# Optimization experiments

Hardware: AMD Instinct MI355X
Metric: run time of the kernel (lower is better)

## Reference

```python
import jax, jax.numpy as jnp
import numpy as np

B, H, S, DK = 2, 16, 2048, 64


def setup_inputs() -> dict:
    key = jax.random.key(0)
    k1, k2, k3, k4 = jax.random.split(key, 4)
    Q = jax.random.normal(k1, (B, H, S, DK), dtype=jnp.float32)
    K = jax.random.normal(k2, (B, H, S, DK), dtype=jnp.float32)
    V = jax.random.normal(k3, (B, H, S, DK), dtype=jnp.float32)
    attn_mask = jax.random.randint(k4, (B, 1, S, S), 0, 2).astype(jnp.bool_)
    return {"Q": Q, "K": K, "V": V, "attn_mask": attn_mask}


def reference(Q, K, V, attn_mask):
    d_k = Q.shape[-1]
    scale = 1.0 / jnp.sqrt(jnp.asarray(d_k, dtype=Q.dtype))
    # scores: [B,H,S,S]
    scores = jnp.einsum('bhqd,bhkd->bhqk', Q, K) * scale
    scores = jnp.where(attn_mask, jnp.asarray(-1e9, dtype=scores.dtype), scores)
    attn = jax.nn.softmax(scores, axis=-1)
    # dropout in eval mode (identity) for deterministic reference
    return jnp.einsum('bhqk,bhkd->bhqd', attn, V)
```

## Files before the change

### kernel.cpp

```cpp
#include <hip/hip_runtime.h>
#include <hip/hip_bf16.h>

#define Bdim 2
#define Hdim 16
#define Sdim 2048
#define Ddim 64
#define KVBLK 64
#define NT (Sdim / KVBLK)
#define WQ 32
#define NWAVE 4
#define QTILE (WQ * NWAVE)
#define QSCL (0.125f * 1.44269504088896f)
#define SCALE 0.125f
#define BUFE 8192
#define VOFF 4096

typedef __bf16 bf16x8 __attribute__((ext_vector_type(8)));
typedef float  f32x4  __attribute__((ext_vector_type(4)));
typedef float  f32x16 __attribute__((ext_vector_type(16)));
typedef unsigned u32x4 __attribute__((ext_vector_type(4)));

__device__ __forceinline__ void gll16(const __bf16* g, __bf16* l) {
  __builtin_amdgcn_global_load_lds(
      (const __attribute__((address_space(1))) void*)g,
      (__attribute__((address_space(3))) void*)l, 16, 0, 0);
}
__device__ __forceinline__ unsigned cvtpk_raw(float lo, float hi) {
  unsigned r;
  asm("v_cvt_pk_bf16_f32 %0, %1, %2" : "=v"(r) : "v"(lo), "v"(hi));
  return r;
}
template <bool SW>
__device__ __forceinline__ unsigned pko(float a, float b) {
  return SW ? cvtpk_raw(b, a) : cvtpk_raw(a, b);
}
__device__ __forceinline__ unsigned cvtpk(float a, float b, bool sw) {
  const float lo = sw ? b : a;
  const float hi = sw ? a : b;
  return cvtpk_raw(lo, hi);
}
template <bool SW>
__device__ __forceinline__ void packAll(const float (&sv0)[16],
                                        const float (&sv1)[16],
                                        unsigned (&pw)[16]) {
#pragma unroll
  for (int ks = 0; ks < 4; ++ks) {
    const int rb = 8 * (ks & 1);
    if (ks < 2) {
      pw[ks * 4 + 0] = pko<SW>(sv0[rb + 0], sv0[rb + 1]);
      pw[ks * 4 + 1] = pko<SW>(sv0[rb + 2], sv0[rb + 3]);
      pw[ks * 4 + 2] = pko<SW>(sv0[rb + 4], sv0[rb + 5]);
      pw[ks * 4 + 3] = pko<SW>(sv0[rb + 6], sv0[rb + 7]);
    } else {
      pw[ks * 4 + 0] = pko<SW>(sv1[rb + 0], sv1[rb + 1]);
      pw[ks * 4 + 1] = pko<SW>(sv1[rb + 2], sv1[rb + 3]);
      pw[ks * 4 + 2] = pko<SW>(sv1[rb + 4], sv1[rb + 5]);
      pw[ks * 4 + 3] = pko<SW>(sv1[rb + 6], sv1[rb + 7]);
    }
  }
}

__global__ __launch_bounds__(256) void pack_mask_kernel(
    const void* __restrict__ mask, unsigned long long* __restrict__ packed) {
  const int nwords = Bdim * Sdim * (Sdim / 64);
  const unsigned* m32 = (const unsigned*)mask;
  const unsigned char* m8 = (const unsigned char*)mask;
  int gid = blockIdx.x * blockDim.x + threadIdx.x;
  int lane = gid & 63;
  int wid = gid >> 6;
  int nwaves = (gridDim.x * blockDim.x) >> 6;

  bool isBytes = __any(m32[lane] > 1u);

  for (int w = wid; w < nwords; w += nwaves) {
    int v = isBytes ? (int)m8[(size_t)w * 64 + lane]
                    : (int)m32[(size_t)w * 64 + lane];
    unsigned long long bal = __ballot(v != 0);
    if (lane == 0) packed[w] = bal;
  }
}

__global__ __launch_bounds__(256) void prep_kv(
    const float* __restrict__ K, const float* __restrict__ V,
    __bf16* __restrict__ Kb, __bf16* __restrict__ Vt) {
  __shared__ __bf16 tile[64][72];
  const int bh = blockIdx.y, st = blockIdx.x;
  const int t = threadIdx.x;
  const int r = t >> 2, c0 = (t & 3) << 4;
  {
    const float* ks = K + ((size_t)bh * Sdim + st * 64 + r) * Ddim + c0;
    bf16x8 o0, o1;
#pragma unroll
    for (int j = 0; j < 8; ++j) o0[j] = (__bf16)ks[j];
#pragma unroll
    for (int j = 0; j < 8; ++j) o1[j] = (__bf16)ks[8 + j];
    __bf16* kd = Kb + ((size_t)bh * Sdim + st * 64 + r) * Ddim + c0;
    *(bf16x8*)kd = o0;
    *(bf16x8*)(kd + 8) = o1;
  }
  {
    const float* vs = V + ((size_t)bh * Sdim + st * 64 + r) * Ddim + c0;
#pragma unroll
    for (int j = 0; j < 16; ++j) tile[r][c0 + j] = (__bf16)vs[j];
  }
  __syncthreads();
  {
    const int d = t >> 2, s0 = (t & 3) << 4;
    __bf16 o[16];
#pragma unroll
    for (int j = 0; j < 16; ++j) o[j] = tile[s0 + j][d];
    __bf16* dst = Vt + ((size_t)bh * Ddim + d) * Sdim + st * 64 + s0;
    *(bf16x8*)dst = *(bf16x8*)&o[0];
    *(bf16x8*)(dst + 8) = *(bf16x8*)&o[8];
  }
}

__global__ __launch_bounds__(256, 2) void attn4(
    const float* __restrict__ Q, const __bf16* __restrict__ Kb,
    const __bf16* __restrict__ Vt,
    const unsigned long long* __restrict__ maskP, float* __restrict__ Out) {
  __shared__ alignas(16) __bf16 sm[3 * BUFE];

  const int tid = threadIdx.x;
  const int lane = tid & 63;
  const int w = tid >> 6;
  const int l31 = lane & 31;
  const int hi = lane >> 5;
  const int rsw = l31 & 7;

  const int bid = blockIdx.x;
  const int bh = bid & 31;
  const int qt = bid >> 5;
  const int b = bh >> 4;
  const int qrow = qt * QTILE + w * WQ + l31;

  const __bf16* Kbase = Kb + (size_t)bh * Sdim * Ddim;
  const __bf16* Vbase = Vt + (size_t)bh * (size_t)Ddim * Sdim;
  const unsigned long long* mp =
      maskP + ((size_t)b * Sdim + qrow) * (Sdim / 64);

  const bool sw = (cvtpk_raw(0.0f, 1.0f) & 0xFFFFu) != 0u;

  bf16x8 qf[4];
  {
    const float* qs = Q + ((size_t)bh * Sdim + qrow) * Ddim;
#pragma unroll
    for (int step = 0; step < 4; ++step) {
      const int d0 = step * 16 + hi * 8;
      float4 a = *(const float4*)(qs + d0);
      float4 c = *(const float4*)(qs + d0 + 4);
      u32x4 f;
      f[0] = cvtpk(a.x * QSCL, a.y * QSCL, sw);
      f[1] = cvtpk(a.z * QSCL, a.w * QSCL, sw);
      f[2] = cvtpk(c.x * QSCL, c.y * QSCL, sw);
      f[3] = cvtpk(c.z * QSCL, c.w * QSCL, sw);
      qf[step] = __builtin_bit_cast(bf16x8, f);
    }
  }

  const int srow = 16 * w + (lane >> 3);
  const int sblk = (lane & 7) ^ ((lane >> 3) & 7);
  const int dstw = w * 1024;

#define STAGE(off_, kt_)                                                        \
  do {                                                                          \
    const __bf16* kp_ = Kbase + ((size_t)(kt_)*KVBLK + srow) * Ddim + sblk * 8; \
    gll16(kp_, &sm[(off_) + dstw]);                                             \
    gll16(kp_ + 8 * Ddim, &sm[(off_) + dstw + 512]);                            \
    const __bf16* vp_ =                                                         \
        Vbase + (size_t)srow * Sdim + (size_t)(kt_)*KVBLK + sblk * 8;           \
    gll16(vp_, &sm[(off_) + VOFF + dstw]);                                      \
    gll16(vp_ + 8 * Sdim, &sm[(off_) + VOFF + dstw + 512]);                     \
  } while (0)

  f32x16 otA = {0,0,0,0,0,0,0,0,0,0,0,0,0,0,0,0};
  f32x16 otB = {0,0,0,0,0,0,0,0,0,0,0,0,0,0,0,0};
  float lrow = 0.f;

  unsigned long long mwCur = mp[0];
  STAGE(0, 0);
  int rdOff = 0, stOff = BUFE;

#pragma unroll 1
  for (int kt = 0; kt < NT; ++kt) {
    const unsigned long long mwNext = mp[kt + 1 < NT ? kt + 1 : NT - 1];
    if (kt + 1 < NT) {
      STAGE(stOff, kt + 1);
      asm volatile("s_waitcnt vmcnt(5)" ::: "memory");
    } else {
      asm volatile("s_waitcnt vmcnt(1)" ::: "memory");
    }
    __builtin_amdgcn_s_barrier();
    __builtin_amdgcn_sched_barrier(0);

    f32x16 st0 = {0,0,0,0,0,0,0,0,0,0,0,0,0,0,0,0};
    f32x16 st1 = {0,0,0,0,0,0,0,0,0,0,0,0,0,0,0,0};
    __builtin_amdgcn_s_setprio(1);
#pragma unroll
    for (int step = 0; step < 4; ++step) {
      bf16x8 kf = *(const bf16x8*)&sm[rdOff + l31 * 64 + (((step * 2 + hi) ^ rsw) << 3)];
      st0 = __builtin_amdgcn_mfma_f32_32x32x16_bf16(kf, qf[step], st0, 0, 0, 0);
    }
#pragma unroll
    for (int step = 0; step < 4; ++step) {
      bf16x8 kf = *(const bf16x8*)&sm[rdOff + (32 + l31) * 64 + (((step * 2 + hi) ^ rsw) << 3)];
      st1 = __builtin_amdgcn_mfma_f32_32x32x16_bf16(kf, qf[step], st1, 0, 0, 0);
    }
    __builtin_amdgcn_s_setprio(0);

    float sv0[16], sv1[16];
    const unsigned w0s = ((unsigned)mwCur) >> (hi * 4);
    const unsigned w1s = ((unsigned)(mwCur >> 32)) >> (hi * 4);
#pragma unroll
    for (int r = 0; r < 16; ++r) {
      const int cr = (r & 3) + 8 * (r >> 2);
      const float e0 = __builtin_amdgcn_exp2f(st0[r]);
      const float e1 = __builtin_amdgcn_exp2f(st1[r]);
      sv0[r] = ((w0s >> cr) & 1u) ? 0.f : e0;
      sv1[r] = ((w1s >> cr) & 1u) ? 0.f : e1;
    }

    float s8[8];
#pragma unroll
    for (int j = 0; j < 8; ++j)
      s8[j] = (sv0[j] + sv0[j + 8]) + (sv1[j] + sv1[j + 8]);
    lrow += ((s8[0] + s8[4]) + (s8[1] + s8[5])) +
            ((s8[2] + s8[6]) + (s8[3] + s8[7]));

    unsigned pw[16];
    if (!sw) packAll<false>(sv0, sv1, pw);
    else     packAll<true>(sv0, sv1, pw);
    bf16x8 pb[4];
#pragma unroll
    for (int ks = 0; ks < 4; ++ks) {
      const unsigned W0 = pw[ks * 4 + 0], W1 = pw[ks * 4 + 1];
      const unsigned X0 = pw[ks * 4 + 2], X1 = pw[ks * 4 + 3];
      const unsigned s1 = hi ? W0 : X0;
      const unsigned s2 = hi ? W1 : X1;
      const unsigned r1 = __shfl_xor(s1, 32, 64);
      const unsigned r2 = __shfl_xor(s2, 32, 64);
      u32x4 wv;
      wv[0] = hi ? r1 : W0;
      wv[1] = hi ? r2 : W1;
      wv[2] = hi ? X0 : r1;
      wv[3] = hi ? X1 : r2;
      pb[ks] = __builtin_bit_cast(bf16x8, wv);
    }

    __builtin_amdgcn_s_setprio(1);
#pragma unroll
    for (int ks = 0; ks < 4; ++ks) {
      bf16x8 vf = *(const bf16x8*)&sm[rdOff + VOFF + l31 * 64 + (((ks * 2 + hi) ^ rsw) << 3)];
      otA = __builtin_amdgcn_mfma_f32_32x32x16_bf16(vf, pb[ks], otA, 0, 0, 0);
    }
#pragma unroll
    for (int ks = 0; ks < 4; ++ks) {
      bf16x8 vf = *(const bf16x8*)&sm[rdOff + VOFF + (32 + l31) * 64 + (((ks * 2 + hi) ^ rsw) << 3)];
      otB = __builtin_amdgcn_mfma_f32_32x32x16_bf16(vf, pb[ks], otB, 0, 0, 0);
    }
    __builtin_amdgcn_s_setprio(0);

    mwCur = mwNext;
    rdOff = stOff;
    stOff = (stOff == 2 * BUFE) ? 0 : stOff + BUFE;
  }
#undef STAGE

  lrow += __shfl_xor(lrow, 32, 64);
  const float inv = 1.f / (lrow + 1e-30f);
  float* orow = Out + ((size_t)bh * Sdim + qrow) * Ddim;
#pragma unroll
  for (int g = 0; g < 4; ++g) {
    const int d0 = 8 * g + 4 * hi;
    float4 va = {otA[4 * g] * inv, otA[4 * g + 1] * inv,
                 otA[4 * g + 2] * inv, otA[4 * g + 3] * inv};
    float4 vb = {otB[4 * g] * inv, otB[4 * g + 1] * inv,
                 otB[4 * g + 2] * inv, otB[4 * g + 3] * inv};
    *(float4*)(orow + d0) = va;
    *(float4*)(orow + 32 + d0) = vb;
  }
}

__global__ __launch_bounds__(256) void attn_fallback(
    const float* __restrict__ Q, const float* __restrict__ K,
    const float* __restrict__ V, const void* __restrict__ maskRaw,
    float* __restrict__ Out) {
  __shared__ alignas(16) __bf16 Kl[KVBLK * Ddim];
  __shared__ alignas(16) __bf16 Vts[Ddim * KVBLK];
  __shared__ alignas(16) __bf16 Pl[4][16 * 64];

  const int tid = threadIdx.x;
  const int lane = tid & 63;
  const int w = tid >> 6;
  const int lhi = lane >> 4;
  const int llo = lane & 15;

  const int qt = blockIdx.x;
  const int bh = blockIdx.y;
  const int b = bh >> 4;
  const int qbase = qt * 64;

  const float* Qp = Q + (size_t)bh * Sdim * Ddim;
  const float* Kp = K + (size_t)bh * Sdim * Ddim;
  const float* Vp = V + (size_t)bh * Sdim * Ddim;

  bool maskBytes = __any(((const unsigned*)maskRaw)[lane] > 1u);

  bf16x8 qf0, qf1;
  {
    const int qr = qbase + w * 16 + llo;
    const float* src = Qp + (size_t)qr * Ddim + lhi * 8;
#pragma unroll
    for (int i = 0; i < 8; ++i) qf0[i] = (__bf16)(src[i] * SCALE);
#pragma unroll
    for (int i = 0; i < 8; ++i) qf1[i] = (__bf16)(src[32 + i] * SCALE);
  }

  f32x4 acc[4] = {{0.f,0.f,0.f,0.f},{0.f,0.f,0.f,0.f},
                  {0.f,0.f,0.f,0.f},{0.f,0.f,0.f,0.f}};
  float mrow[4], lrw[4];
#pragma unroll
  for (int r = 0; r < 4; ++r) { mrow[r] = -3.0e38f; lrw[r] = 0.f; }

  for (int kt = 0; kt < NT; ++kt) {
    __syncthreads();
    {
      int r = tid >> 2;
      int c0 = (tid & 3) << 4;
      const float* ks = Kp + (size_t)(kt * KVBLK + r) * Ddim + c0;
      const float* vs = Vp + (size_t)(kt * KVBLK + r) * Ddim + c0;
      float kv[16], vv[16];
#pragma unroll
      for (int j = 0; j < 4; ++j) {
        *(float4*)(&kv[j * 4]) = *(const float4*)(ks + j * 4);
        *(float4*)(&vv[j * 4]) = *(const float4*)(vs + j * 4);
      }
      const int swzK = (r & 7) << 3;
      bf16x8 k0v, k1v;
#pragma unroll
      for (int j = 0; j < 8; ++j) { k0v[j] = (__bf16)kv[j]; k1v[j] = (__bf16)kv[8 + j]; }
      *(bf16x8*)&Kl[r * 64 + (c0 ^ swzK)] = k0v;
      *(bf16x8*)&Kl[r * 64 + ((c0 + 8) ^ swzK)] = k1v;
#pragma unroll
      for (int j = 0; j < 16; ++j) {
        int d = c0 + j;
        Vts[d * 64 + (r ^ ((d & 7) << 3))] = (__bf16)vv[j];
      }
    }
    __syncthreads();

    float sv[4][4];
#pragma unroll
    for (int cb = 0; cb < 4; ++cb) {
      int krow = cb * 16 + llo;
      int swz = (krow & 7) << 3;
      bf16x8 kf0 = *(const bf16x8*)&Kl[krow * 64 + ((lhi * 8) ^ swz)];
      bf16x8 kf1 = *(const bf16x8*)&Kl[krow * 64 + ((32 + lhi * 8) ^ swz)];
      f32x4 s = {0.f, 0.f, 0.f, 0.f};
      s = __builtin_amdgcn_mfma_f32_16x16x32_bf16(qf0, kf0, s, 0, 0, 0);
      s = __builtin_amdgcn_mfma_f32_16x16x32_bf16(qf1, kf1, s, 0, 0, 0);
#pragma unroll
      for (int r = 0; r < 4; ++r) {
        size_t q = qbase + w * 16 + lhi * 4 + r;
        size_t k = (size_t)kt * KVBLK + cb * 16 + llo;
        size_t idx = ((size_t)b * Sdim + q) * Sdim + k;
        bool masked = maskBytes ? (((const unsigned char*)maskRaw)[idx] != 0)
                                : (((const int*)maskRaw)[idx] != 0);
        sv[cb][r] = masked ? -1e9f : s[r];
      }
    }

    float corr[4], tsum[4];
#pragma unroll
    for (int r = 0; r < 4; ++r) {
      float mx = fmaxf(fmaxf(sv[0][r], sv[1][r]), fmaxf(sv[2][r], sv[3][r]));
#pragma unroll
      for (int off = 1; off < 16; off <<= 1)
        mx = fmaxf(mx, __shfl_xor(mx, off, 64));
      float mnew = fmaxf(mrow[r], mx);
      corr[r] = __expf(mrow[r] - mnew);
      mrow[r] = mnew;
      tsum[r] = 0.f;
    }
#pragma unroll
    for (int cb = 0; cb < 4; ++cb) {
#pragma unroll
      for (int r = 0; r < 4; ++r) {
        float p = __expf(sv[cb][r] - mrow[r]);
        tsum[r] += p;
        int row = lhi * 4 + r;
        int col = cb * 16 + llo;
        Pl[w][row * 64 + (col ^ ((row & 7) << 3))] = (__bf16)p;
      }
    }
#pragma unroll
    for (int r = 0; r < 4; ++r) {
      float s = tsum[r];
#pragma unroll
      for (int off = 1; off < 16; off <<= 1)
        s += __shfl_xor(s, off, 64);
      lrw[r] = lrw[r] * corr[r] + s;
#pragma unroll
      for (int db = 0; db < 4; ++db) acc[db][r] *= corr[r];
    }
    asm volatile("s_waitcnt lgkmcnt(0)" ::: "memory");

    bf16x8 pf0 = *(const bf16x8*)&Pl[w][llo * 64 + ((lhi * 8) ^ ((llo & 7) << 3))];
    bf16x8 pf1 = *(const bf16x8*)&Pl[w][llo * 64 + ((32 + lhi * 8) ^ ((llo & 7) << 3))];
#pragma unroll
    for (int db = 0; db < 4; ++db) {
      int d = db * 16 + llo;
      int swz = (d & 7) << 3;
      bf16x8 vf0 = *(const bf16x8*)&Vts[d * 64 + ((lhi * 8) ^ swz)];
      bf16x8 vf1 = *(const bf16x8*)&Vts[d * 64 + ((32 + lhi * 8) ^ swz)];
      acc[db] = __builtin_amdgcn_mfma_f32_16x16x32_bf16(pf0, vf0, acc[db], 0, 0, 0);
      acc[db] = __builtin_amdgcn_mfma_f32_16x16x32_bf16(pf1, vf1, acc[db], 0, 0, 0);
    }
  }

#pragma unroll
  for (int r = 0; r < 4; ++r) {
    float inv = 1.f / lrw[r];
    int q = qbase + w * 16 + lhi * 4 + r;
    float* dst = Out + ((size_t)bh * Sdim + q) * Ddim + llo;
#pragma unroll
    for (int db = 0; db < 4; ++db) dst[db * 16] = acc[db][r] * inv;
  }
}

extern "C" void kernel_launch(void* const* d_in, const int* in_sizes, int n_in,
                              void* d_out, int out_size, void* d_ws, size_t ws_size,
                              hipStream_t stream) {
  const float* Q = (const float*)d_in[0];
  const float* K = (const float*)d_in[1];
  const float* V = (const float*)d_in[2];
  const void* mask = d_in[3];
  float* out = (float*)d_out;

  const size_t packed_bytes =
      (size_t)Bdim * Sdim * (Sdim / 64) * sizeof(unsigned long long);
  const size_t tensor_bf16 = (size_t)Bdim * Hdim * Sdim * Ddim * 2;

  if (ws_size >= packed_bytes + 2 * tensor_bf16) {
    unsigned long long* packed = (unsigned long long*)d_ws;
    __bf16* Kb = (__bf16*)((char*)d_ws + packed_bytes);
    __bf16* Vt = (__bf16*)((char*)d_ws + packed_bytes + tensor_bf16);
    pack_mask_kernel<<<512, 256, 0, stream>>>(mask, packed);
    prep_kv<<<dim3(Sdim / 64, Bdim * Hdim), 256, 0, stream>>>(K, V, Kb, Vt);
    attn4<<<(Sdim / QTILE) * Bdim * Hdim, 256, 0, stream>>>(Q, Kb, Vt, packed, out);
  } else {
    attn_fallback<<<dim3(Sdim / 64, Bdim * Hdim), 256, 0, stream>>>(Q, K, V, mask, out);
  }
}
```

Baseline: 95.41 us.

## Merge prep kernels and unroll attention loop over four LDS buffers

After: 96.32 us. No clear change (+1.0%).

```diff
diff --git a/kernel.cpp b/kernel.cpp
--- a/kernel.cpp
+++ b/kernel.cpp
@@ -60,32 +60,33 @@
   }
 }
 
-__global__ __launch_bounds__(256) void pack_mask_kernel(
-    const void* __restrict__ mask, unsigned long long* __restrict__ packed) {
-  const int nwords = Bdim * Sdim * (Sdim / 64);
-  const unsigned* m32 = (const unsigned*)mask;
-  const unsigned char* m8 = (const unsigned char*)mask;
-  int gid = blockIdx.x * blockDim.x + threadIdx.x;
-  int lane = gid & 63;
-  int wid = gid >> 6;
-  int nwaves = (gridDim.x * blockDim.x) >> 6;
-
-  bool isBytes = __any(m32[lane] > 1u);
-
-  for (int w = wid; w < nwords; w += nwaves) {
-    int v = isBytes ? (int)m8[(size_t)w * 64 + lane]
-                    : (int)m32[(size_t)w * 64 + lane];
-    unsigned long long bal = __ballot(v != 0);
-    if (lane == 0) packed[w] = bal;
-  }
-}
-
-__global__ __launch_bounds__(256) void prep_kv(
+__global__ __launch_bounds__(256) void prep_all(
+    const void* __restrict__ mask, unsigned long long* __restrict__ packed,
     const float* __restrict__ K, const float* __restrict__ V,
     __bf16* __restrict__ Kb, __bf16* __restrict__ Vt) {
   __shared__ __bf16 tile[64][72];
-  const int bh = blockIdx.y, st = blockIdx.x;
   const int t = threadIdx.x;
+
+  if (blockIdx.x < 512) {
+    const int nwords = Bdim * Sdim * (Sdim / 64);
+    const unsigned* m32 = (const unsigned*)mask;
+    const unsigned char* m8 = (const unsigned char*)mask;
+    int gid = blockIdx.x * 256 + t;
+    int lane = gid & 63;
+    int wid = gid >> 6;
+    const int nwaves = 512 * 256 / 64;
+    bool isBytes = __any(m32[lane] > 1u);
+    for (int w = wid; w < nwords; w += nwaves) {
+      int v = isBytes ? (int)m8[(size_t)w * 64 + lane]
+                      : (int)m32[(size_t)w * 64 + lane];
+      unsigned long long bal = __ballot(v != 0);
+      if (lane == 0) packed[w] = bal;
+    }
+    return;
+  }
+
+  const int idx = blockIdx.x - 512;
+  const int bh = idx >> 5, st = idx & 31;
   const int r = t >> 2, c0 = (t & 3) << 4;
   {
     const float* ks = K + ((size_t)bh * Sdim + st * 64 + r) * Ddim + c0;
@@ -115,11 +116,11 @@
   }
 }
 
-__global__ __launch_bounds__(256, 2) void attn4(
+__global__ __launch_bounds__(256, 2) void attn5(
     const float* __restrict__ Q, const __bf16* __restrict__ Kb,
     const __bf16* __restrict__ Vt,
     const unsigned long long* __restrict__ maskP, float* __restrict__ Out) {
-  __shared__ alignas(16) __bf16 sm[3 * BUFE];
+  __shared__ alignas(16) __bf16 sm[4 * BUFE];
 
   const int tid = threadIdx.x;
   const int lane = tid & 63;
@@ -162,15 +163,12 @@
   const int sblk = (lane & 7) ^ ((lane >> 3) & 7);
   const int dstw = w * 1024;
 
-#define STAGE(off_, kt_)                                                        \
-  do {                                                                          \
-    const __bf16* kp_ = Kbase + ((size_t)(kt_)*KVBLK + srow) * Ddim + sblk * 8; \
-    gll16(kp_, &sm[(off_) + dstw]);                                             \
-    gll16(kp_ + 8 * Ddim, &sm[(off_) + dstw + 512]);                            \
-    const __bf16* vp_ =                                                         \
-        Vbase + (size_t)srow * Sdim + (size_t)(kt_)*KVBLK + sblk * 8;           \
-    gll16(vp_, &sm[(off_) + VOFF + dstw]);                                      \
-    gll16(vp_ + 8 * Sdim, &sm[(off_) + VOFF + dstw + 512]);                     \
+#define STAGE(OFFE, kp_, vp_)                                   \
+  do {                                                          \
+    gll16((kp_), &sm[(OFFE) + dstw]);                           \
+    gll16((kp_) + 8 * Ddim, &sm[(OFFE) + dstw + 512]);          \
+    gll16((vp_), &sm[(OFFE) + VOFF + dstw]);                    \
+    gll16((vp_) + 8 * Sdim, &sm[(OFFE) + VOFF + dstw + 512]);   \
   } while (0)
 
   f32x16 otA = {0,0,0,0,0,0,0,0,0,0,0,0,0,0,0,0};
@@ -178,92 +176,102 @@
   float lrow = 0.f;
 
   unsigned long long mwCur = mp[0];
-  STAGE(0, 0);
-  int rdOff = 0, stOff = BUFE;
+  {
+    const __bf16* kp0 = Kbase + (size_t)srow * Ddim + sblk * 8;
+    const __bf16* vp0 = Vbase + (size_t)srow * Sdim + sblk * 8;
+    STAGE(0, kp0, vp0);
+  }
+  const __bf16* kpS = Kbase + (size_t)(KVBLK + srow) * Ddim + sblk * 8;
+  const __bf16* vpS = Vbase + (size_t)srow * Sdim + KVBLK + sblk * 8;
+
+#define ITER(RD, ST, KTN, LAST)                                                \
+  do {                                                                         \
+    unsigned long long mwNext = 0;                                             \
+    if (!(LAST)) {                                                             \
+      mwNext = mp[(KTN)];                                                      \
+      STAGE((ST) * BUFE, kpS, vpS);                                            \
+      kpS += (size_t)KVBLK * Ddim;                                             \
+      vpS += KVBLK;                                                            \
+      asm volatile("s_waitcnt vmcnt(5)" ::: "memory");                         \
+    } else {                                                                   \
+      asm volatile("s_waitcnt vmcnt(0)" ::: "memory");                         \
+    }                                                                          \
+    __builtin_amdgcn_s_barrier();                                              \
+    __builtin_amdgcn_sched_barrier(0);                                         \
+    f32x16 st0 = {0,0,0,0,0,0,0,0,0,0,0,0,0,0,0,0};                            \
+    f32x16 st1 = {0,0,0,0,0,0,0,0,0,0,0,0,0,0,0,0};                            \
+    __builtin_amdgcn_s_setprio(1);                                             \
+    _Pragma("unroll") for (int step = 0; step < 4; ++step) {                   \
+      bf16x8 kf = *(const bf16x8*)&sm[(RD) * BUFE + l31 * 64 +                 \
+                                      (((step * 2 + hi) ^ rsw) << 3)];         \
+      st0 = __builtin_amdgcn_mfma_f32_32x32x16_bf16(kf, qf[step], st0, 0,0,0); \
+    }                                                                          \
+    _Pragma("unroll") for (int step = 0; step < 4; ++step) {                   \
+      bf16x8 kf = *(const bf16x8*)&sm[(RD) * BUFE + (32 + l31) * 64 +          \
+                                      (((step * 2 + hi) ^ rsw) << 3)];         \
+      st1 = __builtin_amdgcn_mfma_f32_32x32x16_bf16(kf, qf[step], st1, 0,0,0); \
+    }                                                                          \
+    __builtin_amdgcn_s_setprio(0);                                             \
+    float sv0[16], sv1[16];                                                    \
+    const unsigned w0s = ((unsigned)mwCur) >> (hi * 4);                        \
+    const unsigned w1s = ((unsigned)(mwCur >> 32)) >> (hi * 4);                \
+    _Pragma("unroll") for (int r = 0; r < 16; ++r) {                           \
+      const int cr = (r & 3) + 8 * (r >> 2);                                   \
+      const float e0 = __builtin_amdgcn_exp2f(st0[r]);                         \
+      const float e1 = __builtin_amdgcn_exp2f(st1[r]);                         \
+      sv0[r] = ((w0s >> cr) & 1u) ? 0.f : e0;                                  \
+      sv1[r] = ((w1s >> cr) & 1u) ? 0.f : e1;                                  \
+    }                                                                          \
+    float s8[8];                                                               \
+    _Pragma("unroll") for (int j = 0; j < 8; ++j)                              \
+      s8[j] = (sv0[j] + sv0[j + 8]) + (sv1[j] + sv1[j + 8]);                   \
+    lrow += ((s8[0] + s8[4]) + (s8[1] + s8[5])) +                              \
+            ((s8[2] + s8[6]) + (s8[3] + s8[7]));                               \
+    unsigned pw[16];                                                           \
+    if (!sw) packAll<false>(sv0, sv1, pw);                                     \
+    else     packAll<true>(sv0, sv1, pw);                                      \
+    bf16x8 pb[4];                                                              \
+    _Pragma("unroll") for (int ks = 0; ks < 4; ++ks) {                         \
+      const unsigned W0 = pw[ks * 4 + 0], W1 = pw[ks * 4 + 1];                 \
+      const unsigned X0 = pw[ks * 4 + 2], X1 = pw[ks * 4 + 3];                 \
+      const unsigned s1 = hi ? W0 : X0;                                        \
+      const unsigned s2 = hi ? W1 : X1;                                        \
+      const unsigned r1 = __shfl_xor(s1, 32, 64);                              \
+      const unsigned r2 = __shfl_xor(s2, 32, 64);                              \
+      u32x4 wv;                                                                \
+      wv[0] = hi ? r1 : W0;                                                    \
+      wv[1] = hi ? r2 : W1;                                                    \
+      wv[2] = hi ? X0 : r1;                                                    \
+      wv[3] = hi ? X1 : r2;                                                    \
+      pb[ks] = __builtin_bit_cast(bf16x8, wv);                                 \
+    }                                                                          \
+    __builtin_amdgcn_s_setprio(1);                                             \
+    _Pragma("unroll") for (int ks = 0; ks < 4; ++ks) {                         \
+      bf16x8 vf = *(const bf16x8*)&sm[(RD) * BUFE + VOFF + l31 * 64 +          \
+                                      (((ks * 2 + hi) ^ rsw) << 3)];           \
+      otA = __builtin_amdgcn_mfma_f32_32x32x16_bf16(vf, pb[ks], otA, 0,0,0);   \
+    }                                                                          \
+    _Pragma("unroll") for (int ks = 0; ks < 4; ++ks) {                         \
+      bf16x8 vf = *(const bf16x8*)&sm[(RD) * BUFE + VOFF + (32 + l31) * 64 +   \
+                                      (((ks * 2 + hi) ^ rsw) << 3)];           \
+      otB = __builtin_amdgcn_mfma_f32_32x32x16_bf16(vf, pb[ks], otB, 0,0,0);   \
+    }                                                                          \
+    __builtin_amdgcn_s_setprio(0);                                             \
+    if (!(LAST)) mwCur = mwNext;                                               \
+  } while (0)
 
 #pragma unroll 1
-  for (int kt = 0; kt < NT; ++kt) {
-    const unsigned long long mwNext = mp[kt + 1 < NT ? kt + 1 : NT - 1];
-    if (kt + 1 < NT) {
-      STAGE(stOff, kt + 1);
-      asm volatile("s_waitcnt vmcnt(5)" ::: "memory");
-    } else {
-      asm volatile("s_waitcnt vmcnt(1)" ::: "memory");
-    }
-    __builtin_amdgcn_s_barrier();
-    __builtin_amdgcn_sched_barrier(0);
-
-    f32x16 st0 = {0,0,0,0,0,0,0,0,0,0,0,0,0,0,0,0};
-    f32x16 st1 = {0,0,0,0,0,0,0,0,0,0,0,0,0,0,0,0};
-    __builtin_amdgcn_s_setprio(1);
-#pragma unroll
-    for (int step = 0; step < 4; ++step) {
-      bf16x8 kf = *(const bf16x8*)&sm[rdOff + l31 * 64 + (((step * 2 + hi) ^ rsw) << 3)];
-      st0 = __builtin_amdgcn_mfma_f32_32x32x16_bf16(kf, qf[step], st0, 0, 0, 0);
-    }
-#pragma unroll
-    for (int step = 0; step < 4; ++step) {
-      bf16x8 kf = *(const bf16x8*)&sm[rdOff + (32 + l31) * 64 + (((step * 2 + hi) ^ rsw) << 3)];
-      st1 = __builtin_amdgcn_mfma_f32_32x32x16_bf16(kf, qf[step], st1, 0, 0, 0);
-    }
-    __builtin_amdgcn_s_setprio(0);
-
-    float sv0[16], sv1[16];
-    const unsigned w0s = ((unsigned)mwCur) >> (hi * 4);
-    const unsigned w1s = ((unsigned)(mwCur >> 32)) >> (hi * 4);
-#pragma unroll
-    for (int r = 0; r < 16; ++r) {
-      const int cr = (r & 3) + 8 * (r >> 2);
-      const float e0 = __builtin_amdgcn_exp2f(st0[r]);
-      const float e1 = __builtin_amdgcn_exp2f(st1[r]);
-      sv0[r] = ((w0s >> cr) & 1u) ? 0.f : e0;
-      sv1[r] = ((w1s >> cr) & 1u) ? 0.f : e1;
-    }
-
-    float s8[8];
-#pragma unroll
-    for (int j = 0; j < 8; ++j)
-      s8[j] = (sv0[j] + sv0[j + 8]) + (sv1[j] + sv1[j + 8]);
-    lrow += ((s8[0] + s8[4]) + (s8[1] + s8[5])) +
-            ((s8[2] + s8[6]) + (s8[3] + s8[7]));
-
-    unsigned pw[16];
-    if (!sw) packAll<false>(sv0, sv1, pw);
-    else     packAll<true>(sv0, sv1, pw);
-    bf16x8 pb[4];
-#pragma unroll
-    for (int ks = 0; ks < 4; ++ks) {
-      const unsigned W0 = pw[ks * 4 + 0], W1 = pw[ks * 4 + 1];
-      const unsigned X0 = pw[ks * 4 + 2], X1 = pw[ks * 4 + 3];
-      const unsigned s1 = hi ? W0 : X0;
-      const unsigned s2 = hi ? W1 : X1;
-      const unsigned r1 = __shfl_xor(s1, 32, 64);
-      const unsigned r2 = __shfl_xor(s2, 32, 64);
-      u32x4 wv;
-      wv[0] = hi ? r1 : W0;
-      wv[1] = hi ? r2 : W1;
-      wv[2] = hi ? X0 : r1;
-      wv[3] = hi ? X1 : r2;
-      pb[ks] = __builtin_bit_cast(bf16x8, wv);
-    }
-
-    __builtin_amdgcn_s_setprio(1);
-#pragma unroll
-    for (int ks = 0; ks < 4; ++ks) {
-      bf16x8 vf = *(const bf16x8*)&sm[rdOff + VOFF + l31 * 64 + (((ks * 2 + hi) ^ rsw) << 3)];
-      otA = __builtin_amdgcn_mfma_f32_32x32x16_bf16(vf, pb[ks], otA, 0, 0, 0);
-    }
-#pragma unroll
-    for (int ks = 0; ks < 4; ++ks) {
-      bf16x8 vf = *(const bf16x8*)&sm[rdOff + VOFF + (32 + l31) * 64 + (((ks * 2 + hi) ^ rsw) << 3)];
-      otB = __builtin_amdgcn_mfma_f32_32x32x16_bf16(vf, pb[ks], otB, 0, 0, 0);
-    }
-    __builtin_amdgcn_s_setprio(0);
-
-    mwCur = mwNext;
-    rdOff = stOff;
-    stOff = (stOff == 2 * BUFE) ? 0 : stOff + BUFE;
-  }
+  for (int g = 0; g < 7; ++g) {
+    ITER(0, 1, 4 * g + 1, false);
+    ITER(1, 2, 4 * g + 2, false);
+    ITER(2, 3, 4 * g + 3, false);
+    ITER(3, 0, 4 * g + 4, false);
+  }
+  ITER(0, 1, 29, false);
+  ITER(1, 2, 30, false);
+  ITER(2, 3, 31, false);
+  ITER(3, 0, 0, true);
+#undef ITER
 #undef STAGE
 
   lrow += __shfl_xor(lrow, 32, 64);
@@ -445,9 +453,9 @@
     unsigned long long* packed = (unsigned long long*)d_ws;
     __bf16* Kb = (__bf16*)((char*)d_ws + packed_bytes);
     __bf16* Vt = (__bf16*)((char*)d_ws + packed_bytes + tensor_bf16);
-    pack_mask_kernel<<<512, 256, 0, stream>>>(mask, packed);
-    prep_kv<<<dim3(Sdim / 64, Bdim * Hdim), 256, 0, stream>>>(K, V, Kb, Vt);
-    attn4<<<(Sdim / QTILE) * Bdim * Hdim, 256, 0, stream>>>(Q, Kb, Vt, packed, out);
+    prep_all<<<512 + Bdim * Hdim * (Sdim / 64), 256, 0, stream>>>(
+        mask, packed, K, V, Kb, Vt);
+    attn5<<<(Sdim / QTILE) * Bdim * Hdim, 256, 0, stream>>>(Q, Kb, Vt, packed, out);
   } else {
     attn_fallback<<<dim3(Sdim / 64, Bdim * Hdim), 256, 0, stream>>>(Q, K, V, mask, out);
   }
```
